# Performance work log

Measured on AMD Instinct MI355X. Metric: run time of the kernel, lower is better.

Reference implementation:

```python
import jax, jax.numpy as jnp
import numpy as np

N, NFEAT, NHID, NCLASS, NHEADS = 4096, 512, 64, 40, 8
ALPHA = 0.2
NEG = -9e15


def setup_inputs() -> dict:
    key = jax.random.key(0)
    ks = jax.random.split(key, 6)
    x = jax.random.normal(ks[0], (N, NFEAT), dtype=jnp.float32)
    adj = jax.random.randint(ks[1], (2, N, N), 0, 2, dtype=jnp.int32)
    # Xavier-ish scaled params
    W1 = jax.random.normal(ks[2], (NHEADS, NFEAT, NHID), dtype=jnp.float32) * (1.0 / np.sqrt(NFEAT))
    a1 = jax.random.normal(ks[3], (NHEADS, 2, NHID), dtype=jnp.float32) * (1.0 / np.sqrt(2 * NHID))
    Wo = jax.random.normal(ks[4], (NHEADS * NHID, NCLASS), dtype=jnp.float32) * (1.0 / np.sqrt(NHEADS * NHID))
    ao = jax.random.normal(ks[5], (2, NCLASS), dtype=jnp.float32) * (1.0 / np.sqrt(2 * NCLASS))
    return {"x": x, "adj": adj, "W1": W1, "a1": a1, "Wo": Wo, "ao": ao}


def _gat_layer(h, adj_mask, W, a_src, a_dst, concat):
    # h: [N,F]; W: [...,F,F']; a_src/a_dst: [...,F']
    if W.ndim == 3:  # multi-head: [H,F,F']
        Wh = jnp.einsum('nf,hfd->hnd', h, W)              # [H,N,F']
        f1 = jnp.einsum('hnd,hd->hn', Wh, a_src)           # [H,N]
        f2 = jnp.einsum('hnd,hd->hn', Wh, a_dst)
        e = jax.nn.leaky_relu(f1[:, :, None] + f2[:, None, :], ALPHA)  # [H,N,N]
        e = jnp.where(adj_mask[None], e, NEG)
        att = jax.nn.softmax(e, axis=-1)
        out = jnp.einsum('hnm,hmd->hnd', att, Wh)          # [H,N,F']
    else:
        Wh = h @ W                                         # [N,F']
        f1 = Wh @ a_src
        f2 = Wh @ a_dst
        e = jax.nn.leaky_relu(f1[:, None] + f2[None, :], ALPHA)
        e = jnp.where(adj_mask, e, NEG)
        att = jax.nn.softmax(e, axis=-1)
        out = att @ Wh
    return jax.nn.elu(out) if concat else out


def reference(x, adj, W1, a1, Wo, ao):
    adj1 = adj[1] > 0
    adj0 = adj[0] > 0
    # layer 1: NHEADS heads, concat=True
    h = _gat_layer(x, adj1, W1, a1[:, 0], a1[:, 1], concat=True)   # [H,N,NHID]
    h = jnp.transpose(h, (1, 0, 2)).reshape(x.shape[0], -1)        # [N, H*NHID]
    # output layer: concat=False, then outer ELU + log_softmax
    out = _gat_layer(h, adj0, Wo, ao[0], ao[1], concat=False)      # [N, NCLASS]
    out = jax.nn.elu(out)
    return jax.nn.log_softmax(out, axis=1)
```

## Files before the change

kernel.cpp:

```cpp
#include <hip/hip_runtime.h>
#include <hip/hip_bf16.h>

#define N      4096
#define NFEAT  512
#define NHID   64
#define NHEADS 8
#define NCLASS 40
#define ALPHA  0.2f
#define LOG2E  1.44269504f

typedef unsigned short u16;
typedef unsigned int   u32;
typedef __attribute__((ext_vector_type(8))) short bf16x8;
typedef __attribute__((ext_vector_type(4))) float f32x4;

__device__ __forceinline__ float b2f(u16 u) {
    return __uint_as_float(((u32)u) << 16);
}
__device__ __forceinline__ u32 rnd_hi(float f) {
    u32 u = __float_as_uint(f);
    return u + 0x7FFFu + ((u >> 16) & 1u);
}
__device__ __forceinline__ u32 pk2(float lo, float hi) {
    __hip_bfloat162 h = __float22bfloat162_rn(make_float2(lo, hi));
    return *(u32*)&h;
}
__device__ __forceinline__ u16 f2b(float f) {
    return (u16)(rnd_hi(f) >> 16);
}
__device__ __forceinline__ float mexp(int m, float t) {
    return m ? __builtin_amdgcn_exp2f(fmaxf(t, ALPHA * t)) : 0.f;
}
__device__ __forceinline__ bf16x8 ones_frag() {
    union { u16 u[8]; bf16x8 v; } o;
    #pragma unroll
    for (int j = 0; j < 8; ++j) o.u[j] = 0x3F80;
    return o.v;
}
__device__ __forceinline__ void gload_lds16(const u16* g, u16* l) {
    __builtin_amdgcn_global_load_lds(
        (const __attribute__((address_space(1))) void*)g,
        (__attribute__((address_space(3))) void*)l,
        16, 0, 0);
}

__global__ __launch_bounds__(256) void kcx(const float* __restrict__ x,
                                           u16* __restrict__ xb) {
    const int g = blockIdx.x * 256 + threadIdx.x;
    const size_t base = (size_t)g * 8;
    float4 v0 = *(const float4*)&x[base];
    float4 v1 = *(const float4*)&x[base + 4];
    uint4 o;
    o.x = pk2(v0.x, v0.y); o.y = pk2(v0.z, v0.w);
    o.z = pk2(v1.x, v1.y); o.w = pk2(v1.z, v1.w);
    *(uint4*)&xb[base] = o;
}

__global__ __launch_bounds__(256) void kcw(const float* __restrict__ W1,
                                           u16* __restrict__ W1b) {
    __shared__ float ts[64 * 68];
    const int t  = threadIdx.x;
    const int f0 = blockIdx.x * 64;
    const int h  = blockIdx.y;
    #pragma unroll
    for (int i = 0; i < 4; ++i) {
        int flat = t + 256 * i;
        int row = flat >> 4;
        int c4  = (flat & 15) * 4;
        *(float4*)&ts[row * 68 + c4] =
            *(const float4*)&W1[((size_t)h * 512 + f0 + row) * 64 + c4];
    }
    __syncthreads();
    const int d  = t >> 2;
    const int fs = (t & 3) * 16;
    u32 p[8];
    #pragma unroll
    for (int j = 0; j < 8; ++j)
        p[j] = pk2(ts[(fs + 2 * j) * 68 + d], ts[(fs + 2 * j + 1) * 68 + d]);
    u32* dst = (u32*)&W1b[((size_t)(h * 64 + d)) * 512 + f0 + fs];
    *(uint4*)dst       = make_uint4(p[0], p[1], p[2], p[3]);
    *(uint4*)(dst + 4) = make_uint4(p[4], p[5], p[6], p[7]);
}

__global__ __launch_bounds__(256, 4) void k1m_gemm1(const u16* __restrict__ xb,
                                                    const u16* __restrict__ W1b,
                                                    const float* __restrict__ a1,
                                                    u16* __restrict__ Wh1T,
                                                    float* __restrict__ F1,
                                                    float* __restrict__ F2) {
    __shared__ __align__(16) u16 xs[2][64 * 64];
    __shared__ __align__(16) u16 wvs[2][64 * 64];
    const int t    = threadIdx.x;
    const int n0   = blockIdx.x * 64;
    const int h    = blockIdx.y;
    const int lane = t & 63;
    const int l15  = lane & 15;
    const int q    = lane >> 4;
    const int wv   = t >> 6;
    const int wrow = wv * 16;
    const int lsub = lane >> 3;
    const int slot = lane & 7;
    const int xb7  = l15 & 7;

    const u16* gx[2];
    const u16* gw[2];
    #pragma unroll
    for (int i = 0; i < 2; ++i) {
        const int r  = wv * 16 + i * 8 + lsub;
        const int sc = (slot ^ lsub) * 8;
        gx[i] = xb  + (size_t)(n0 + r) * 512 + sc;
        gw[i] = W1b + ((size_t)(h * 64 + r)) * 512 + sc;
    }

    f32x4 acc[4];
    #pragma unroll
    for (int df = 0; df < 4; ++df)
        #pragma unroll
        for (int r = 0; r < 4; ++r) acc[df][r] = 0.f;

#define K1_DMA(P, F0)                                                          \
    {                                                                          \
        _Pragma("unroll")                                                      \
        for (int i = 0; i < 2; ++i) {                                          \
            gload_lds16(gx[i] + (F0), &xs[P][(wv * 16 + i * 8) * 64]);         \
            gload_lds16(gw[i] + (F0), &wvs[P][(wv * 16 + i * 8) * 64]);        \
        }                                                                      \
    }
#define K1_MFMA(P)                                                             \
    {                                                                          \
        _Pragma("unroll")                                                      \
        for (int ks = 0; ks < 2; ++ks) {                                       \
            const int sl = ((ks * 4 + q) ^ xb7) * 8;                           \
            bf16x8 a = *(const bf16x8*)&xs[P][(wrow + l15) * 64 + sl];         \
            _Pragma("unroll")                                                  \
            for (int df = 0; df < 4; ++df) {                                   \
                bf16x8 b = *(const bf16x8*)&wvs[P][(df * 16 + l15) * 64 + sl]; \
                acc[df] = __builtin_amdgcn_mfma_f32_16x16x32_bf16(a, b, acc[df], 0, 0, 0); \
            }                                                                  \
        }                                                                      \
    }

    K1_DMA(0, 0)
    __syncthreads();
    for (int f0 = 0; f0 < 512; f0 += 128) {
        K1_DMA(1, f0 + 64)
        K1_MFMA(0)
        __syncthreads();
        if (f0 + 128 < 512)
            K1_DMA(0, f0 + 128)
        K1_MFMA(1)
        __syncthreads();
    }
#undef K1_DMA
#undef K1_MFMA

    #pragma unroll
    for (int df = 0; df < 4; ++df) {
        uint2 o;
        o.x = pk2(acc[df][0], acc[df][1]);
        o.y = pk2(acc[df][2], acc[df][3]);
        *(uint2*)&Wh1T[((size_t)(h * 64 + df * 16 + l15)) * 4096 + n0 + wrow + q * 4] = o;
    }
    float a1v[4], a2v[4];
    #pragma unroll
    for (int df = 0; df < 4; ++df) {
        a1v[df] = a1[h * 128 + df * 16 + l15];
        a2v[df] = a1[h * 128 + 64 + df * 16 + l15];
    }
    #pragma unroll
    for (int r = 0; r < 4; ++r) {
        float s1 = 0.f, s2 = 0.f;
        #pragma unroll
        for (int df = 0; df < 4; ++df) {
            s1 += acc[df][r] * a1v[df];
            s2 += acc[df][r] * a2v[df];
        }
        #pragma unroll
        for (int off = 8; off >= 1; off >>= 1) {
            s1 += __shfl_xor(s1, off);
            s2 += __shfl_xor(s2, off);
        }
        if (l15 == 0) {
            int n = n0 + wrow + q * 4 + r;
            F1[h * 4096 + n] = s1 * LOG2E;
            F2[h * 4096 + n] = s2 * LOG2E;
        }
    }
}

__global__ __launch_bounds__(256, 4) void k3_attn1(const int* __restrict__ adj1,
                                                   const u16* __restrict__ Wh1T,
                                                   const float* __restrict__ F1,
                                                   const float* __restrict__ F2,
                                                   float* __restrict__ h1) {
    __shared__ __align__(16) u16 wbf[32 * 136];
    __shared__ __align__(16) u16 whT[64 * 128];
    __shared__ float f1s[32];
    __shared__ float zs[32];
    const int t     = threadIdx.x;
    const int n0    = blockIdx.x * 32;
    const int h     = blockIdx.y;
    const int lane  = t & 63;
    const int l15   = lane & 15;
    const int q     = lane >> 4;
    const int wv    = t >> 6;
    const int rb    = (wv & 1) * 16;
    const int dh    = wv >> 1;
    const int c4    = (t & 31) * 4;
    const int rg    = t >> 5;
    const bf16x8 bones = ones_frag();
    if (t < 32) f1s[t] = F1[h * N + n0 + t];

    const int lsub = lane >> 4;
    const int slot = lane & 15;
    const u16* gsrc[4];
    #pragma unroll
    for (int i = 0; i < 4; ++i) {
        int row_l = wv * 16 + i * 4 + lsub;
        int sc    = (slot ^ ((i * 4 + lsub) & 7)) * 8;
        gsrc[i] = Wh1T + ((size_t)(h * 64 + row_l)) * 4096 + sc;
    }
    u16* ldst = &whT[wv * 2048];
    const int xb7 = l15 & 7;

    f32x4 accd[2], accz;
    #pragma unroll
    for (int j = 0; j < 2; ++j)
        #pragma unroll
        for (int r = 0; r < 4; ++r) accd[j][r] = 0.f;
    #pragma unroll
    for (int r = 0; r < 4; ++r) accz[r] = 0.f;

    int4 aprev[4];
    #pragma unroll
    for (int i = 0; i < 4; ++i)
        aprev[i] = *(const int4*)&adj1[(size_t)(n0 + rg + 8 * i) * N + c4];
    float4 f2n = *(const float4*)&F2[h * N + c4];
    __syncthreads();

    for (int m0 = 0; m0 < 4096; m0 += 128) {
        #pragma unroll
        for (int i = 0; i < 4; ++i)
            gload_lds16(gsrc[i] + m0, ldst + i * 512);
        const float4 F2v = f2n;
        const int mn = (m0 + 128 < 4096) ? m0 + 128 : 0;
        f2n = *(const float4*)&F2[h * N + mn + c4];
        #pragma unroll
        for (int i = 0; i < 4; ++i) {
            const int rr = rg + 8 * i;
            int4 a4 = aprev[i];
            aprev[i] = *(const int4*)&adj1[(size_t)(n0 + rr) * N + mn + c4];
            float f1v = f1s[rr];
            float w0 = mexp(a4.x, f1v + F2v.x);
            float w1 = mexp(a4.y, f1v + F2v.y);
            float w2 = mexp(a4.z, f1v + F2v.z);
            float w3 = mexp(a4.w, f1v + F2v.w);
            uint2 pk;
            pk.x = pk2(w0, w1);
            pk.y = pk2(w2, w3);
            *(uint2*)&wbf[rr * 136 + c4] = pk;
        }
        __syncthreads();
        #pragma unroll
        for (int ks = 0; ks < 4; ++ks) {
            int k0 = ks * 32 + q * 8;
            bf16x8 a = *(const bf16x8*)&wbf[(rb + l15) * 136 + k0];
            #pragma unroll
            for (int j = 0; j < 2; ++j) {
                const int df = dh * 2 + j;
                bf16x8 b = *(const bf16x8*)
                    &whT[(df * 16 + l15) * 128 + (((ks * 4 + q) ^ xb7) * 8)];
                accd[j] = __builtin_amdgcn_mfma_f32_16x16x32_bf16(a, b, accd[j], 0, 0, 0);
            }
            if (dh == 0)
                accz = __builtin_amdgcn_mfma_f32_16x16x32_bf16(a, bones, accz, 0, 0, 0);
        }
        __syncthreads();
    }
    if (dh == 0 && l15 == 0) {
        #pragma unroll
        for (int r = 0; r < 4; ++r) zs[rb + q * 4 + r] = accz[r];
    }
    __syncthreads();
    #pragma unroll
    for (int r = 0; r < 4; ++r) {
        const int nl = rb + q * 4 + r;
        const float z = fmaxf(zs[nl], 1e-30f);
        #pragma unroll
        for (int j = 0; j < 2; ++j) {
            float v = accd[j][r] / z;
            v = v > 0.f ? v : __expf(v) - 1.f;
            h1[(size_t)(n0 + nl) * 512 + h * 64 + (dh * 2 + j) * 16 + l15] = v;
        }
    }
}

__global__ __launch_bounds__(256) void k4_gemm2(const float* __restrict__ h1,
                                                const float* __restrict__ Wo,
                                                const float* __restrict__ ao,
                                                float* __restrict__ F1o,
                                                float* __restrict__ F2o,
                                                u16* __restrict__ Wh2T) {
    const int t = threadIdx.x;
    const int c = t & 63;
    const int n = blockIdx.x * 4 + (t >> 6);
    float acc = 0.f;
    if (c < NCLASS) {
        const float* hrow = &h1[(size_t)n * 512];
        #pragma unroll 8
        for (int f = 0; f < 512; ++f)
            acc += hrow[f] * Wo[f * NCLASS + c];
        Wh2T[(size_t)c * 4096 + n] = f2b(acc);
    }
    float s1 = (c < NCLASS) ? acc * ao[c] : 0.f;
    float s2 = (c < NCLASS) ? acc * ao[NCLASS + c] : 0.f;
    #pragma unroll
    for (int off = 32; off >= 1; off >>= 1) {
        s1 += __shfl_xor(s1, off);
        s2 += __shfl_xor(s2, off);
    }
    if (c == 0) {
        F1o[n] = s1 * LOG2E;
        F2o[n] = s2 * LOG2E;
    }
}

__global__ __launch_bounds__(256, 5) void k5a_attn2(const int* __restrict__ adj0,
                                                    const u16* __restrict__ Wh2T,
                                                    const float* __restrict__ F1o,
                                                    const float* __restrict__ F2o,
                                                    float* __restrict__ pacc,
                                                    float* __restrict__ pz) {
    __shared__ __align__(16) u16 wbf[64 * 136];
    __shared__ __align__(16) u16 whT[48 * 128];
    __shared__ float f1s[64];
    const int t     = threadIdx.x;
    const int n0    = blockIdx.x * 64;
    const int chunk = blockIdx.y;
    const int mbase = chunk * 256;
    const int lane  = t & 63;
    const int l15   = lane & 15;
    const int q     = lane >> 4;
    const int wrow  = (t >> 6) * 16;
    const int c4    = (t & 31) * 4;
    const int rg    = t >> 5;
    const bf16x8 bones = ones_frag();
    if (t < 64) f1s[t] = F1o[n0 + t];
    #pragma unroll
    for (int i = 0; i < 4; ++i)
        whT[40 * 128 + t + 256 * i] = 0;

    const int wv   = t >> 6;
    const int lsub = lane >> 4;
    const int slot = lane & 15;
    const int ninst = (wv < 2) ? 4 : ((wv == 2) ? 2 : 0);
    const u16* gsrc[4];
    #pragma unroll
    for (int i = 0; i < 4; ++i) {
        int row_l = wv * 16 + i * 4 + lsub;
        int rl    = (row_l < 40) ? row_l : 0;
        int sc    = (slot ^ ((i * 4 + lsub) & 7)) * 8;
        gsrc[i] = Wh2T + (size_t)rl * 4096 + sc;
    }
    u16* ldst = &whT[wv * 2048];
    const int xb7 = l15 & 7;

    f32x4 acc[4];
    #pragma unroll
    for (int df = 0; df < 4; ++df)
        #pragma unroll
        for (int r = 0; r < 4; ++r) acc[df][r] = 0.f;

    int4 aprev[8];
    #pragma unroll
    for (int i = 0; i < 8; ++i)
        aprev[i] = *(const int4*)&adj0[(size_t)(n0 + rg + 8 * i) * N + mbase + c4];
    __syncthreads();

    #pragma unroll
    for (int mt = 0; mt < 2; ++mt) {
        const int m0 = mbase + mt * 128;
        #pragma unroll
        for (int i = 0; i < 4; ++i)
            if (i < ninst)
                gload_lds16(gsrc[i] + m0, ldst + i * 512);
        float4 F2v = *(const float4*)&F2o[m0 + c4];
        #pragma unroll
        for (int i = 0; i < 8; ++i) {
            int rr = rg + 8 * i;
            int4 a4 = aprev[i];
            float f1v = f1s[rr];
            float w0 = mexp(a4.x, f1v + F2v.x);
            float w1 = mexp(a4.y, f1v + F2v.y);
            float w2 = mexp(a4.z, f1v + F2v.z);
            float w3 = mexp(a4.w, f1v + F2v.w);
            uint2 pk;
            pk.x = pk2(w0, w1);
            pk.y = pk2(w2, w3);
            *(uint2*)&wbf[rr * 136 + c4] = pk;
        }
        int mn = mbase + ((mt + 1) & 1) * 128;
        #pragma unroll
        for (int i = 0; i < 8; ++i)
            aprev[i] = *(const int4*)&adj0[(size_t)(n0 + rg + 8 * i) * N + mn + c4];
        __syncthreads();
        #pragma unroll
        for (int ks = 0; ks < 4; ++ks) {
            int k0 = ks * 32 + q * 8;
            bf16x8 a = *(const bf16x8*)&wbf[(wrow + l15) * 136 + k0];
            #pragma unroll
            for (int df = 0; df < 3; ++df) {
                bf16x8 b = *(const bf16x8*)
                    &whT[(df * 16 + l15) * 128 + (((ks * 4 + q) ^ xb7) * 8)];
                acc[df] = __builtin_amdgcn_mfma_f32_16x16x32_bf16(a, b, acc[df], 0, 0, 0);
            }
            acc[3] = __builtin_amdgcn_mfma_f32_16x16x32_bf16(a, bones, acc[3], 0, 0, 0);
        }
        __syncthreads();
    }
    #pragma unroll
    for (int r = 0; r < 4; ++r) {
        int n = n0 + wrow + q * 4 + r;
        if (l15 == 0) pz[(size_t)chunk * N + n] = acc[3][r];
        #pragma unroll
        for (int df = 0; df < 3; ++df) {
            int c = df * 16 + l15;
            if (c < NCLASS)
                pacc[((size_t)chunk * N + n) * NCLASS + c] = acc[df][r];
        }
    }
}

__global__ __launch_bounds__(256) void k5b_final(const float* __restrict__ pacc,
                                                 const float* __restrict__ pz,
                                                 float* __restrict__ out) {
    const int t = threadIdx.x;
    const int lane = t & 63;
    const int n = blockIdx.x * 4 + (t >> 6);
    float s = 0.f, Z = 0.f;
    #pragma unroll
    for (int ch = 0; ch < 16; ++ch) {
        Z += pz[(size_t)ch * N + n];
        if (lane < NCLASS) s += pacc[(size_t)(ch * N + n) * NCLASS + lane];
    }
    float v;
    if (lane < NCLASS) {
        v = s / fmaxf(Z, 1e-30f);
        v = v > 0.f ? v : __expf(v) - 1.f;
    } else {
        v = -INFINITY;
    }
    float mx = v;
    #pragma unroll
    for (int off = 32; off >= 1; off >>= 1) mx = fmaxf(mx, __shfl_xor(mx, off));
    float ex = (lane < NCLASS) ? __expf(v - mx) : 0.f;
    #pragma unroll
    for (int off = 32; off >= 1; off >>= 1) ex += __shfl_xor(ex, off);
    float lse = mx + __logf(ex);
    if (lane < NCLASS) out[(size_t)n * NCLASS + lane] = v - lse;
}

extern "C" void kernel_launch(void* const* d_in, const int* in_sizes, int n_in,
                              void* d_out, int out_size, void* d_ws, size_t ws_size,
                              hipStream_t stream) {
    const float* x   = (const float*)d_in[0];
    const int*   adj = (const int*)d_in[1];
    const float* W1  = (const float*)d_in[2];
    const float* a1  = (const float*)d_in[3];
    const float* Wo  = (const float*)d_in[4];
    const float* ao  = (const float*)d_in[5];

    float* ws    = (float*)d_ws;
    float* h1    = ws;
    float* F1    = h1 + 2097152;
    float* F2    = F1 + 32768;
    float* F1o   = F2 + 32768;
    float* F2o   = F1o + 4096;
    float* pz    = F2o + 4096;
    float* pz1   = pz + 65536;
    u16*   Wh1T  = (u16*)(pz1 + 65536);
    u16*   Wh2T  = Wh1T + 2097152;
    float* R     = (float*)(Wh2T + 163840);
    u16*   xb    = (u16*)R;
    u16*   W1b   = xb + 2097152;
    float* pacc  = R;

    const int* adj0 = adj;
    const int* adj1 = adj + (size_t)N * N;

    hipLaunchKernelGGL(kcx,       dim3(1024),   dim3(256), 0, stream, x, xb);
    hipLaunchKernelGGL(kcw,       dim3(8, 8),   dim3(256), 0, stream, W1, W1b);
    hipLaunchKernelGGL(k1m_gemm1, dim3(64, 8),  dim3(256), 0, stream, xb, W1b, a1, Wh1T, F1, F2);
    hipLaunchKernelGGL(k3_attn1,  dim3(128, 8), dim3(256), 0, stream, adj1, Wh1T, F1, F2, h1);
    hipLaunchKernelGGL(k4_gemm2,  dim3(1024),   dim3(256), 0, stream, h1, Wo, ao, F1o, F2o, Wh2T);
    hipLaunchKernelGGL(k5a_attn2, dim3(64, 16), dim3(256), 0, stream, adj0, Wh2T, F1o, F2o, pacc, pz);
    hipLaunchKernelGGL(k5b_final, dim3(1024),   dim3(256), 0, stream, pacc, pz, (float*)d_out);
}
```

Baseline: 307.7 us.

## Double-buffer attention kernel with 64-wide chunks and one barrier per step

Restructures the layer-1 attention kernel so the adjacency-to-weights conversion and Wh tile DMA for the next 64-column chunk go into a second LDS buffer while MFMAs consume the current one. This cuts barriers from two per 128 columns to one per 64, and keeps F1 in registers instead of shared memory. The goal is to overlap the exp/pack work with matrix work. In exchange it adds register pressure from two-deep prefetch and runs more loop iterations with smaller chunks.

```diff
diff --git a/kernel.cpp b/kernel.cpp
--- a/kernel.cpp
+++ b/kernel.cpp
@@ -126,7 +126,7 @@
             gload_lds16(gw[i] + (F0), &wvs[P][(wv * 16 + i * 8) * 64]);        \
         }                                                                      \
     }
-#define K1_MFMA(P)                                                             \
+#define K1_MFMA(P)                                                            \
     {                                                                          \
         _Pragma("unroll")                                                      \
         for (int ks = 0; ks < 2; ++ks) {                                       \
@@ -193,36 +193,39 @@
                                                    const float* __restrict__ F1,
                                                    const float* __restrict__ F2,
                                                    float* __restrict__ h1) {
-    __shared__ __align__(16) u16 wbf[32 * 136];
-    __shared__ __align__(16) u16 whT[64 * 128];
-    __shared__ float f1s[32];
+    __shared__ __align__(16) u16 wbf[2][32 * 72];
+    __shared__ __align__(16) u16 whT[2][64 * 64];
     __shared__ float zs[32];
-    const int t     = threadIdx.x;
-    const int n0    = blockIdx.x * 32;
-    const int h     = blockIdx.y;
-    const int lane  = t & 63;
-    const int l15   = lane & 15;
-    const int q     = lane >> 4;
-    const int wv    = t >> 6;
-    const int rb    = (wv & 1) * 16;
-    const int dh    = wv >> 1;
-    const int c4    = (t & 31) * 4;
-    const int rg    = t >> 5;
+    const int t    = threadIdx.x;
+    const int n0   = blockIdx.x * 32;
+    const int h    = blockIdx.y;
+    const int lane = t & 63;
+    const int l15  = lane & 15;
+    const int q    = lane >> 4;
+    const int wv   = t >> 6;
+    const int rb   = (wv & 1) * 16;
+    const int dh   = wv >> 1;
+    const int rg2  = t >> 4;
+    const int c4h  = (t & 15) * 4;
     const bf16x8 bones = ones_frag();
-    if (t < 32) f1s[t] = F1[h * N + n0 + t];
-
-    const int lsub = lane >> 4;
-    const int slot = lane & 15;
-    const u16* gsrc[4];
-    #pragma unroll
-    for (int i = 0; i < 4; ++i) {
-        int row_l = wv * 16 + i * 4 + lsub;
-        int sc    = (slot ^ ((i * 4 + lsub) & 7)) * 8;
-        gsrc[i] = Wh1T + ((size_t)(h * 64 + row_l)) * 4096 + sc;
-    }
-    u16* ldst = &whT[wv * 2048];
+
+    const float f1a = F1[h * N + n0 + rg2];
+    const float f1b = F1[h * N + n0 + rg2 + 16];
+
+    const int lsub = lane >> 3;
+    const int slot = lane & 7;
+    const u16* gsrc[2];
+    #pragma unroll
+    for (int i = 0; i < 2; ++i) {
+        const int r = wv * 16 + i * 8 + lsub;
+        gsrc[i] = Wh1T + ((size_t)(h * 64 + r)) * 4096 + (slot ^ lsub) * 8;
+    }
     const int xb7 = l15 & 7;
 
+    const int*   adjA = adj1 + (size_t)(n0 + rg2) * N + c4h;
+    const int*   adjB = adj1 + (size_t)(n0 + rg2 + 16) * N + c4h;
+    const float* f2p  = F2 + (size_t)h * N + c4h;
+
     f32x4 accd[2], accz;
     #pragma unroll
     for (int j = 0; j < 2; ++j)
@@ -231,52 +234,67 @@
     #pragma unroll
     for (int r = 0; r < 4; ++r) accz[r] = 0.f;
 
-    int4 aprev[4];
-    #pragma unroll
-    for (int i = 0; i < 4; ++i)
-        aprev[i] = *(const int4*)&adj1[(size_t)(n0 + rg + 8 * i) * N + c4];
-    float4 f2n = *(const float4*)&F2[h * N + c4];
+    int4   ajA0 = *(const int4*)(adjA);
+    int4   ajB0 = *(const int4*)(adjB);
+    float4 f2r0 = *(const float4*)(f2p);
+    #pragma unroll
+    for (int i = 0; i < 2; ++i)
+        gload_lds16(gsrc[i], &whT[0][(wv * 16 + i * 8) * 64]);
+    int4   ajA1 = *(const int4*)(adjA + 64);
+    int4   ajB1 = *(const int4*)(adjB + 64);
+    float4 f2r1 = *(const float4*)(f2p + 64);
+    {
+        uint2 pa, pb;
+        pa.x = pk2(mexp(ajA0.x, f1a + f2r0.x), mexp(ajA0.y, f1a + f2r0.y));
+        pa.y = pk2(mexp(ajA0.z, f1a + f2r0.z), mexp(ajA0.w, f1a + f2r0.w));
+        pb.x = pk2(mexp(ajB0.x, f1b + f2r0.x), mexp(ajB0.y, f1b + f2r0.y));
+        pb.y = pk2(mexp(ajB0.z, f1b + f2r0.z), mexp(ajB0.w, f1b + f2r0.w));
+        *(uint2*)&wbf[0][rg2 * 72 + c4h]        = pa;
+        *(uint2*)&wbf[0][(rg2 + 16) * 72 + c4h] = pb;
+    }
     __syncthreads();
 
-    for (int m0 = 0; m0 < 4096; m0 += 128) {
-        #pragma unroll
-        for (int i = 0; i < 4; ++i)
-            gload_lds16(gsrc[i] + m0, ldst + i * 512);
-        const float4 F2v = f2n;
-        const int mn = (m0 + 128 < 4096) ? m0 + 128 : 0;
-        f2n = *(const float4*)&F2[h * N + mn + c4];
-        #pragma unroll
-        for (int i = 0; i < 4; ++i) {
-            const int rr = rg + 8 * i;
-            int4 a4 = aprev[i];
-            aprev[i] = *(const int4*)&adj1[(size_t)(n0 + rr) * N + mn + c4];
-            float f1v = f1s[rr];
-            float w0 = mexp(a4.x, f1v + F2v.x);
-            float w1 = mexp(a4.y, f1v + F2v.y);
-            float w2 = mexp(a4.z, f1v + F2v.z);
-            float w3 = mexp(a4.w, f1v + F2v.w);
-            uint2 pk;
-            pk.x = pk2(w0, w1);
-            pk.y = pk2(w2, w3);
-            *(uint2*)&wbf[rr * 136 + c4] = pk;
-        }
-        __syncthreads();
-        #pragma unroll
-        for (int ks = 0; ks < 4; ++ks) {
-            int k0 = ks * 32 + q * 8;
-            bf16x8 a = *(const bf16x8*)&wbf[(rb + l15) * 136 + k0];
-            #pragma unroll
-            for (int j = 0; j < 2; ++j) {
-                const int df = dh * 2 + j;
-                bf16x8 b = *(const bf16x8*)
-                    &whT[(df * 16 + l15) * 128 + (((ks * 4 + q) ^ xb7) * 8)];
-                accd[j] = __builtin_amdgcn_mfma_f32_16x16x32_bf16(a, b, accd[j], 0, 0, 0);
-            }
-            if (dh == 0)
-                accz = __builtin_amdgcn_mfma_f32_16x16x32_bf16(a, bones, accz, 0, 0, 0);
-        }
-        __syncthreads();
-    }
+    int mh = 0;
+#define K3_STEP(RP, MGA, MGB, MGF, PFA, PFB, PFF)                               \
+    {                                                                           \
+        const int mh1 = (mh + 64) & 4095;                                       \
+        const int mh2 = (mh + 128) & 4095;                                      \
+        _Pragma("unroll")                                                       \
+        for (int i = 0; i < 2; ++i)                                             \
+            gload_lds16(gsrc[i] + mh1, &whT[(RP) ^ 1][(wv * 16 + i * 8) * 64]); \
+        int4 a4 = MGA; int4 b4 = MGB; float4 fv = MGF;                          \
+        PFA = *(const int4*)(adjA + mh2);                                       \
+        PFB = *(const int4*)(adjB + mh2);                                       \
+        PFF = *(const float4*)(f2p + mh2);                                      \
+        uint2 pa, pb;                                                           \
+        pa.x = pk2(mexp(a4.x, f1a + fv.x), mexp(a4.y, f1a + fv.y));             \
+        pa.y = pk2(mexp(a4.z, f1a + fv.z), mexp(a4.w, f1a + fv.w));             \
+        pb.x = pk2(mexp(b4.x, f1b + fv.x), mexp(b4.y, f1b + fv.y));             \
+        pb.y = pk2(mexp(b4.z, f1b + fv.z), mexp(b4.w, f1b + fv.w));             \
+        *(uint2*)&wbf[(RP) ^ 1][rg2 * 72 + c4h]        = pa;                    \
+        *(uint2*)&wbf[(RP) ^ 1][(rg2 + 16) * 72 + c4h] = pb;                    \
+        _Pragma("unroll")                                                       \
+        for (int ks = 0; ks < 2; ++ks) {                                        \
+            bf16x8 a = *(const bf16x8*)&wbf[RP][(rb + l15) * 72 + ks * 32 + q * 8]; \
+            _Pragma("unroll")                                                   \
+            for (int j = 0; j < 2; ++j) {                                       \
+                bf16x8 b = *(const bf16x8*)                                     \
+                    &whT[RP][((dh * 2 + j) * 16 + l15) * 64 + (((ks * 4 + q) ^ xb7) * 8)]; \
+                accd[j] = __builtin_amdgcn_mfma_f32_16x16x32_bf16(a, b, accd[j], 0, 0, 0); \
+            }                                                                   \
+            if (dh == 0)                                                        \
+                accz = __builtin_amdgcn_mfma_f32_16x16x32_bf16(a, bones, accz, 0, 0, 0); \
+        }                                                                       \
+        __syncthreads();                                                        \
+        mh = mh1;                                                               \
+    }
+
+    for (int it = 0; it < 32; ++it) {
+        K3_STEP(0, ajA1, ajB1, f2r1, ajA0, ajB0, f2r0)
+        K3_STEP(1, ajA0, ajB0, f2r0, ajA1, ajB1, f2r1)
+    }
+#undef K3_STEP
+
     if (dh == 0 && l15 == 0) {
         #pragma unroll
         for (int r = 0; r < 4; ++r) zs[rb + q * 4 + r] = accz[r];
```

Result: no change. 308.8 us (+0.4%).

## Retile second attention kernel to 32-row blocks with split class-column waves

Applied to the files above, without the earlier changes.

The layer-2 attention kernel now processes 32 query rows per block over 512 key columns (8 chunks instead of 16). The four waves split the work into two row halves and two groups of class columns instead of one row stripe each. The adjacency prefetch for the next tile is interleaved with the exp computation, and the F2 loads are double-buffered. This halves the partial-sum traffic read by the final reduction and cuts the MFMA work per wave, at the cost of fewer rows sharing each staged Wh2T tile and a loop that is no longer unrolled.

```diff
diff --git a/kernel.cpp b/kernel.cpp
--- a/kernel.cpp
+++ b/kernel.cpp
@@ -126,7 +126,7 @@
             gload_lds16(gw[i] + (F0), &wvs[P][(wv * 16 + i * 8) * 64]);        \
         }                                                                      \
     }
-#define K1_MFMA(P)                                                             \
+#define K1_MFMA(P)                                                            \
     {                                                                          \
         _Pragma("unroll")                                                      \
         for (int ks = 0; ks < 2; ++ks) {                                       \
@@ -325,32 +325,33 @@
     }
 }
 
-__global__ __launch_bounds__(256, 5) void k5a_attn2(const int* __restrict__ adj0,
+__global__ __launch_bounds__(256, 4) void k5a_attn2(const int* __restrict__ adj0,
                                                     const u16* __restrict__ Wh2T,
                                                     const float* __restrict__ F1o,
                                                     const float* __restrict__ F2o,
                                                     float* __restrict__ pacc,
                                                     float* __restrict__ pz) {
-    __shared__ __align__(16) u16 wbf[64 * 136];
+    __shared__ __align__(16) u16 wbf[32 * 136];
     __shared__ __align__(16) u16 whT[48 * 128];
-    __shared__ float f1s[64];
+    __shared__ float f1s[32];
     const int t     = threadIdx.x;
-    const int n0    = blockIdx.x * 64;
+    const int n0    = blockIdx.x * 32;
     const int chunk = blockIdx.y;
-    const int mbase = chunk * 256;
+    const int mbase = chunk * 512;
     const int lane  = t & 63;
     const int l15   = lane & 15;
     const int q     = lane >> 4;
-    const int wrow  = (t >> 6) * 16;
+    const int wv    = t >> 6;
+    const int rb    = (wv & 1) * 16;
+    const int dh    = wv >> 1;
     const int c4    = (t & 31) * 4;
     const int rg    = t >> 5;
     const bf16x8 bones = ones_frag();
-    if (t < 64) f1s[t] = F1o[n0 + t];
+    if (t < 32) f1s[t] = F1o[n0 + t];
     #pragma unroll
     for (int i = 0; i < 4; ++i)
         whT[40 * 128 + t + 256 * i] = 0;
 
-    const int wv   = t >> 6;
     const int lsub = lane >> 4;
     const int slot = lane & 15;
     const int ninst = (wv < 2) ? 4 : ((wv == 2) ? 2 : 0);
@@ -365,30 +366,31 @@
     u16* ldst = &whT[wv * 2048];
     const int xb7 = l15 & 7;
 
-    f32x4 acc[4];
-    #pragma unroll
-    for (int df = 0; df < 4; ++df)
-        #pragma unroll
-        for (int r = 0; r < 4; ++r) acc[df][r] = 0.f;
-
-    int4 aprev[8];
-    #pragma unroll
-    for (int i = 0; i < 8; ++i)
+    f32x4 acc0, acc1, accz;
+    #pragma unroll
+    for (int r = 0; r < 4; ++r) { acc0[r] = 0.f; acc1[r] = 0.f; accz[r] = 0.f; }
+
+    int4 aprev[4];
+    #pragma unroll
+    for (int i = 0; i < 4; ++i)
         aprev[i] = *(const int4*)&adj0[(size_t)(n0 + rg + 8 * i) * N + mbase + c4];
+    float4 f2n = *(const float4*)&F2o[mbase + c4];
     __syncthreads();
 
-    #pragma unroll
-    for (int mt = 0; mt < 2; ++mt) {
-        const int m0 = mbase + mt * 128;
+    for (int it = 0; it < 4; ++it) {
+        const int m0 = mbase + it * 128;
         #pragma unroll
         for (int i = 0; i < 4; ++i)
             if (i < ninst)
                 gload_lds16(gsrc[i] + m0, ldst + i * 512);
-        float4 F2v = *(const float4*)&F2o[m0 + c4];
-        #pragma unroll
-        for (int i = 0; i < 8; ++i) {
-            int rr = rg + 8 * i;
+        const float4 F2v = f2n;
+        const int mn = (it < 3) ? m0 + 128 : mbase;
+        f2n = *(const float4*)&F2o[mn + c4];
+        #pragma unroll
+        for (int i = 0; i < 4; ++i) {
+            const int rr = rg + 8 * i;
             int4 a4 = aprev[i];
+            aprev[i] = *(const int4*)&adj0[(size_t)(n0 + rr) * N + mn + c4];
             float f1v = f1s[rr];
             float w0 = mexp(a4.x, f1v + F2v.x);
             float w1 = mexp(a4.y, f1v + F2v.y);
@@ -399,34 +401,35 @@
             pk.y = pk2(w2, w3);
             *(uint2*)&wbf[rr * 136 + c4] = pk;
         }
-        int mn = mbase + ((mt + 1) & 1) * 128;
-        #pragma unroll
-        for (int i = 0; i < 8; ++i)
-            aprev[i] = *(const int4*)&adj0[(size_t)(n0 + rg + 8 * i) * N + mn + c4];
         __syncthreads();
         #pragma unroll
         for (int ks = 0; ks < 4; ++ks) {
             int k0 = ks * 32 + q * 8;
-            bf16x8 a = *(const bf16x8*)&wbf[(wrow + l15) * 136 + k0];
-            #pragma unroll
-            for (int df = 0; df < 3; ++df) {
-                bf16x8 b = *(const bf16x8*)
-                    &whT[(df * 16 + l15) * 128 + (((ks * 4 + q) ^ xb7) * 8)];
-                acc[df] = __builtin_amdgcn_mfma_f32_16x16x32_bf16(a, b, acc[df], 0, 0, 0);
+            bf16x8 a = *(const bf16x8*)&wbf[(rb + l15) * 136 + k0];
+            const int sl = (((ks * 4 + q) ^ xb7) * 8);
+            if (dh == 0) {
+                bf16x8 b0 = *(const bf16x8*)&whT[(0 * 16 + l15) * 128 + sl];
+                acc0 = __builtin_amdgcn_mfma_f32_16x16x32_bf16(a, b0, acc0, 0, 0, 0);
+                accz = __builtin_amdgcn_mfma_f32_16x16x32_bf16(a, bones, accz, 0, 0, 0);
+            } else {
+                bf16x8 b1 = *(const bf16x8*)&whT[(1 * 16 + l15) * 128 + sl];
+                acc0 = __builtin_amdgcn_mfma_f32_16x16x32_bf16(a, b1, acc0, 0, 0, 0);
+                bf16x8 b2 = *(const bf16x8*)&whT[(2 * 16 + l15) * 128 + sl];
+                acc1 = __builtin_amdgcn_mfma_f32_16x16x32_bf16(a, b2, acc1, 0, 0, 0);
             }
-            acc[3] = __builtin_amdgcn_mfma_f32_16x16x32_bf16(a, bones, acc[3], 0, 0, 0);
         }
         __syncthreads();
     }
     #pragma unroll
     for (int r = 0; r < 4; ++r) {
-        int n = n0 + wrow + q * 4 + r;
-        if (l15 == 0) pz[(size_t)chunk * N + n] = acc[3][r];
-        #pragma unroll
-        for (int df = 0; df < 3; ++df) {
-            int c = df * 16 + l15;
-            if (c < NCLASS)
-                pacc[((size_t)chunk * N + n) * NCLASS + c] = acc[df][r];
+        const int n = n0 + rb + q * 4 + r;
+        const size_t base = ((size_t)chunk * N + n) * NCLASS;
+        if (dh == 0) {
+            if (l15 == 0) pz[(size_t)chunk * N + n] = accz[r];
+            pacc[base + l15] = acc0[r];
+        } else {
+            pacc[base + 16 + l15] = acc0[r];
+            if (l15 < 8) pacc[base + 32 + l15] = acc1[r];
         }
     }
 }
@@ -439,7 +442,7 @@
     const int n = blockIdx.x * 4 + (t >> 6);
     float s = 0.f, Z = 0.f;
     #pragma unroll
-    for (int ch = 0; ch < 16; ++ch) {
+    for (int ch = 0; ch < 8; ++ch) {
         Z += pz[(size_t)ch * N + n];
         if (lane < NCLASS) s += pacc[(size_t)(ch * N + n) * NCLASS + lane];
     }
@@ -493,6 +496,6 @@
     hipLaunchKernelGGL(k1m_gemm1, dim3(64, 8),  dim3(256), 0, stream, xb, W1b, a1, Wh1T, F1, F2);
     hipLaunchKernelGGL(k3_attn1,  dim3(128, 8), dim3(256), 0, stream, adj1, Wh1T, F1, F2, h1);
     hipLaunchKernelGGL(k4_gemm2,  dim3(1024),   dim3(256), 0, stream, h1, Wo, ao, F1o, F2o, Wh2T);
-    hipLaunchKernelGGL(k5a_attn2, dim3(64, 16), dim3(256), 0, stream, adj0, Wh2T, F1o, F2o, pacc, pz);
+    hipLaunchKernelGGL(k5a_attn2, dim3(128, 8), dim3(256), 0, stream, adj0, Wh2T, F1o, F2o, pacc, pz);
     hipLaunchKernelGGL(k5b_final, dim3(1024),   dim3(256), 0, stream, pacc, pz, (float*)d_out);
 }
```

New measurement: 302.1 us. About the same (-1.8%).
